# Optimization experiments

Measured on AMD Instinct MI355X. Metric: run time of the kernel, lower is better.

Reference implementation:

```python
import jax, jax.numpy as jnp
import numpy as np

VOCAB, D, B, T = 32000, 1024, 4, 2048

def setup_inputs() -> dict:
    key = jax.random.key(0)
    ks = jax.random.split(key, 7)
    std = 0.01  # model initializes all weights with std=0.01
    return {
        "x": jax.random.randint(ks[0], (B, T), 0, VOCAB),
        "emb_w": jax.random.normal(ks[1], (VOCAB, D), jnp.float32) * std,
        "wq": jax.random.normal(ks[2], (D, D), jnp.float32) * std,
        "wk": jax.random.normal(ks[3], (D, D), jnp.float32) * std,
        "wv": jax.random.normal(ks[4], (D, D), jnp.float32) * std,
        "wo": jax.random.normal(ks[5], (D, D), jnp.float32) * std,
        "wout": jax.random.normal(ks[6], (VOCAB, D), jnp.float32) * std,
    }

def fhe_act(x):
    # polynomial activation: 0.1*x^2 + 0.1*x
    return x * x * 0.1 + x * 0.1

def reference(x, emb_w, wq, wk, wv, wo, wout):
    h = emb_w[x] * 0.01                                 # [B,T,D]
    q = (h @ wq.T) * 0.01                               # [B,T,D]
    k = (h @ wk.T) * 0.01                               # [B,T,D]
    v = (h @ wv.T) * 0.1                                # [B,T,D]
    attn = jnp.einsum('btd,bsd->bts', q, k) * 0.01      # [B,T,T] full (no causal mask)
    attn = fhe_act(attn)
    out = jnp.einsum('bts,bsd->btd', attn, v) * 0.01    # [B,T,D]
    out = (out @ wo.T) * 0.1                            # [B,T,D]
    logits = out @ wout.T                               # [B,T,VOCAB]
    return logits
```

## Files before the change

### kernel.cpp

```cpp
#include <hip/hip_runtime.h>


typedef __bf16 bf16_t;
typedef __bf16 bf16x8 __attribute__((ext_vector_type(8)));
typedef __bf16 bf16x4 __attribute__((ext_vector_type(4)));
typedef float  f32x4  __attribute__((ext_vector_type(4)));

#define VOCAB 32000
#define DIM   1024
#define BATCH 4
#define SEQ   2048
#define BT    (BATCH*SEQ)

__device__ __forceinline__ void gload_lds16(const void* g, void* l) {
    __builtin_amdgcn_global_load_lds(
        (const __attribute__((address_space(1))) void*)g,
        (__attribute__((address_space(3))) void*)l,
        16, 0, 0);
}

__global__ void cast_f32_to_bf16(const float* __restrict__ in, bf16_t* __restrict__ out, int n4) {
    int i = blockIdx.x * blockDim.x + threadIdx.x;
    if (i < n4) {
        float4 v = ((const float4*)in)[i];
        bf16x4 o;
        o.x = (bf16_t)v.x; o.y = (bf16_t)v.y; o.z = (bf16_t)v.z; o.w = (bf16_t)v.w;
        ((bf16x4*)out)[i] = o;
    }
}

__global__ void embed_gather(const int* __restrict__ x, const float* __restrict__ emb,
                             bf16_t* __restrict__ h) {
    const int tok = blockIdx.x;
    const int row = x[tok];
    const float4* src = (const float4*)(emb + (long)row * DIM);
    bf16x4* dst = (bf16x4*)(h + (long)tok * DIM);
    int j = threadIdx.x;
    float4 v = src[j];
    bf16x4 o;
    o.x = (bf16_t)(v.x * 0.01f); o.y = (bf16_t)(v.y * 0.01f);
    o.z = (bf16_t)(v.z * 0.01f); o.w = (bf16_t)(v.w * 0.01f);
    dst[j] = o;
}

template<int ACT, typename CT>
__global__ __launch_bounds__(256) void gemm_bt(
    const bf16_t* __restrict__ A, const bf16_t* __restrict__ B, CT* __restrict__ C,
    int M, int N, int K, long sA, long sB, long sC, float scale)
{
    __shared__ __align__(16) bf16_t lsA[128 * 32];
    __shared__ __align__(16) bf16_t lsB[128 * 32];

    const int bz = blockIdx.z;
    A += (long)bz * sA;  B += (long)bz * sB;  C += (long)bz * sC;

    const int tm = blockIdx.y, tn = blockIdx.x;
    const int t = threadIdx.x;
    const int lane = t & 63, wave = t >> 6;
    const int wm = (wave >> 1) * 64;
    const int wn = (wave & 1) * 64;

    const int srow = t >> 2;
    const int scol = (t & 3) * 8;
    const bf16_t* gA = A + (long)(tm * 128 + srow) * K + scol;
    const bf16_t* gB = B + (long)(tn * 128 + srow) * K + scol;
    bf16_t* lA = &lsA[srow * 32 + scol];
    bf16_t* lB = &lsB[srow * 32 + scol];

    f32x4 acc[4][4];
#pragma unroll
    for (int i = 0; i < 4; ++i)
#pragma unroll
        for (int j = 0; j < 4; ++j)
            acc[i][j] = (f32x4){0.f, 0.f, 0.f, 0.f};

    const int arow = lane & 15;
    const int acol = (lane >> 4) * 8;

    for (int k0 = 0; k0 < K; k0 += 32) {
        __syncthreads();
        gload_lds16(gA + k0,                lA);
        gload_lds16(gA + k0 + 64 * (long)K, lA + 64 * 32);
        gload_lds16(gB + k0,                lB);
        gload_lds16(gB + k0 + 64 * (long)K, lB + 64 * 32);
        __syncthreads();

        bf16x8 af[4], bfr[4];
#pragma unroll
        for (int i = 0; i < 4; ++i) {
            af[i]  = *(const bf16x8*)&lsA[(wm + i * 16 + arow) * 32 + acol];
            bfr[i] = *(const bf16x8*)&lsB[(wn + i * 16 + arow) * 32 + acol];
        }
#pragma unroll
        for (int i = 0; i < 4; ++i)
#pragma unroll
            for (int j = 0; j < 4; ++j)
                acc[i][j] = __builtin_amdgcn_mfma_f32_16x16x32_bf16(af[i], bfr[j], acc[i][j], 0, 0, 0);
    }

    const int crow0 = tm * 128 + wm + (lane >> 4) * 4;
    const int ccol0 = tn * 128 + wn + (lane & 15);
#pragma unroll
    for (int i = 0; i < 4; ++i)
#pragma unroll
        for (int j = 0; j < 4; ++j)
#pragma unroll
            for (int r = 0; r < 4; ++r) {
                float s = acc[i][j][r] * scale;
                if (ACT) s = s * s * 0.1f + s * 0.1f;
                C[(long)(crow0 + i * 16 + r) * N + (ccol0 + j * 16)] = (CT)s;
            }
}

__global__ __launch_bounds__(512, 2) void gemm_bt_256(
    const bf16_t* __restrict__ A, const bf16_t* __restrict__ B, float* __restrict__ C,
    int N, int K, float scale)
{
    __shared__ __align__(16) char smem[131072];
    char* const sm = smem;

    const int lin = blockIdx.x;
    const int xcd = lin & 7, jj = lin >> 3;
    const int tm = xcd * 4 + (jj & 3);
    const int tn = jj >> 2;
    const long trow0 = (long)tm * 256, tcol0 = (long)tn * 256;

    const int tid  = threadIdx.x;
    const int lane = tid & 63;
    const int wave = tid >> 6;
    const int wm = wave >> 2;
    const int wn = wave & 3;
    const int lr = lane & 15;
    const int ko2 = (lane >> 4) * 16;
    const int rbase = lr * 64 + (ko2 ^ (((lr >> 1) & 3) << 4));

    const int o0 = tid * 16, o1 = 8192 + tid * 16;
    int sr0, sc0, sr1, sc1;
    {
        int ol = o0 ^ (((o0 >> 7) & 3) << 4);
        sr0 = ((ol >> 10) >> 1) * 16 + ((ol >> 6) & 15);
        sc0 = ((ol >> 10) & 1) * 32 + ((ol & 63) >> 1);
        ol = o1 ^ (((o1 >> 7) & 3) << 4);
        sr1 = ((ol >> 10) >> 1) * 16 + ((ol >> 6) & 15);
        sc1 = ((ol >> 10) & 1) * 32 + ((ol & 63) >> 1);
    }

    const bf16_t* Abase = A + trow0 * K;
    const bf16_t* Bbase = B + tcol0 * K;

#define STAGE_HT(gbase, kt, half, ldsh) do {                                          \
    gload_lds16((gbase) + (long)((half) * 128 + sr0) * K + ((kt) * 64 + sc0), (ldsh) + o0); \
    gload_lds16((gbase) + (long)((half) * 128 + sr1) * K + ((kt) * 64 + sc1), (ldsh) + o1); \
} while (0)

    f32x4 acc[8][4];
#pragma unroll
    for (int i = 0; i < 8; ++i)
#pragma unroll
        for (int j = 0; j < 4; ++j)
            acc[i][j] = (f32x4){0.f, 0.f, 0.f, 0.f};

#define PHASE(mh, nh, ...) do {                                                       \
    bf16x8 af_[4][2], bv_[2][2];                                                      \
    _Pragma("unroll")                                                                 \
    for (int i_ = 0; i_ < 4; ++i_) {                                                  \
        _Pragma("unroll")                                                             \
        for (int ks_ = 0; ks_ < 2; ++ks_)                                             \
            af_[i_][ks_] = *(const bf16x8*)(ldsA + (mh) * 16384 +                     \
                               ((wm * 4 + i_) * 2 + ks_) * 1024 + rbase);             \
    }                                                                                 \
    _Pragma("unroll")                                                                 \
    for (int j_ = 0; j_ < 2; ++j_) {                                                  \
        _Pragma("unroll")                                                             \
        for (int ks_ = 0; ks_ < 2; ++ks_)                                             \
            bv_[j_][ks_] = *(const bf16x8*)(ldsB + (nh) * 16384 +                     \
                               ((wn * 2 + j_) * 2 + ks_) * 1024 + rbase);             \
    }                                                                                 \
    __VA_ARGS__;                                                                      \
    asm volatile("s_barrier" ::: "memory");                                           \
    asm volatile("s_waitcnt lgkmcnt(0)" ::: "memory");                                \
    __builtin_amdgcn_s_setprio(1);                                                    \
    _Pragma("unroll")                                                                 \
    for (int i_ = 0; i_ < 4; ++i_)                                                    \
        _Pragma("unroll")                                                             \
        for (int j_ = 0; j_ < 2; ++j_)                                                \
            _Pragma("unroll")                                                         \
            for (int ks_ = 0; ks_ < 2; ++ks_)                                         \
                acc[(mh) * 4 + i_][(nh) * 2 + j_] =                                   \
                    __builtin_amdgcn_mfma_f32_16x16x32_bf16(                          \
                        af_[i_][ks_], bv_[j_][ks_],                                   \
                        acc[(mh) * 4 + i_][(nh) * 2 + j_], 0, 0, 0);                  \
    __builtin_amdgcn_s_setprio(0);                                                    \
} while (0)

    {
        char* a0 = sm;
        char* b0 = sm + 32768;
        char* a1 = sm + 65536;
        char* b1 = sm + 65536 + 32768;
        STAGE_HT(Abase, 0, 0, a0);
        STAGE_HT(Bbase, 0, 0, b0);
        STAGE_HT(Abase, 0, 1, a0 + 16384);
        STAGE_HT(Bbase, 0, 1, b0 + 16384);
        STAGE_HT(Abase, 1, 0, a1);
        STAGE_HT(Bbase, 1, 0, b1);
        asm volatile("s_waitcnt vmcnt(4)" ::: "memory");
        asm volatile("s_barrier" ::: "memory");
    }

    const int NT = K / 64;
    for (int t = 0; t < NT; ++t) {
        const int buf = t & 1;
        char* ldsA  = sm + buf * 65536;
        char* ldsB  = ldsA + 32768;
        char* ldsAn = sm + (buf ^ 1) * 65536;
        char* ldsBn = ldsAn + 32768;

        PHASE(0, 0,
              if (t + 1 < NT) {
                  STAGE_HT(Abase, t + 1, 1, ldsAn + 16384);
                  STAGE_HT(Bbase, t + 1, 1, ldsBn + 16384);
              });
        asm volatile("s_barrier" ::: "memory");

        PHASE(0, 1, );
        asm volatile("s_barrier" ::: "memory");

        PHASE(1, 0,
              if (t + 2 < NT) { STAGE_HT(Abase, t + 2, 0, ldsA); });
        asm volatile("s_barrier" ::: "memory");

        PHASE(1, 1,
              if (t + 2 < NT) { STAGE_HT(Bbase, t + 2, 0, ldsB); });
        if (t + 2 < NT) { asm volatile("s_waitcnt vmcnt(4)" ::: "memory"); }
        else            { asm volatile("s_waitcnt vmcnt(0)" ::: "memory"); }
        asm volatile("s_barrier" ::: "memory");
    }

    const int erow = (lane >> 4) * 4;
    const int ecol = lane & 15;
#pragma unroll
    for (int mh = 0; mh < 2; ++mh)
#pragma unroll
        for (int i = 0; i < 4; ++i)
#pragma unroll
            for (int nh = 0; nh < 2; ++nh)
#pragma unroll
                for (int j = 0; j < 2; ++j)
#pragma unroll
                    for (int r = 0; r < 4; ++r) {
                        long row = trow0 + mh * 128 + wm * 64 + i * 16 + erow + r;
                        long col = tcol0 + nh * 128 + wn * 32 + j * 16 + ecol;
                        C[row * N + col] = acc[mh * 4 + i][nh * 2 + j][r] * scale;
                    }
#undef PHASE
#undef STAGE_HT
}

extern "C" void kernel_launch(void* const* d_in, const int* in_sizes, int n_in,
                              void* d_out, int out_size, void* d_ws, size_t ws_size,
                              hipStream_t stream) {
    const int*   x    = (const int*)d_in[0];
    const float* emb  = (const float*)d_in[1];
    const float* wq   = (const float*)d_in[2];
    const float* wk   = (const float*)d_in[3];
    const float* wv   = (const float*)d_in[4];
    const float* wo   = (const float*)d_in[5];
    const float* wout = (const float*)d_in[6];
    float* logits = (float*)d_out;

    char* ws = (char*)d_ws;
    size_t off = 0;
    auto alloc = [&](size_t bytes) {
        char* p = ws + off;
        off += (bytes + 255) & ~(size_t)255;
        return p;
    };
    bf16_t* hb    = (bf16_t*)alloc((size_t)BT * DIM * 2);
    bf16_t* qb    = (bf16_t*)alloc((size_t)BT * DIM * 2);
    bf16_t* kb    = (bf16_t*)alloc((size_t)BT * DIM * 2);
    bf16_t* vtb   = (bf16_t*)alloc((size_t)BATCH * DIM * SEQ * 2);
    bf16_t* attnb = (bf16_t*)alloc((size_t)BATCH * SEQ * SEQ * 2);
    bf16_t* o1b   = (bf16_t*)alloc((size_t)BT * DIM * 2);
    bf16_t* o2b   = (bf16_t*)alloc((size_t)BT * DIM * 2);
    bf16_t* wqb   = (bf16_t*)alloc((size_t)DIM * DIM * 2);
    bf16_t* wkb   = (bf16_t*)alloc((size_t)DIM * DIM * 2);
    bf16_t* wvb   = (bf16_t*)alloc((size_t)DIM * DIM * 2);
    bf16_t* wob   = (bf16_t*)alloc((size_t)DIM * DIM * 2);
    bf16_t* woutb = (bf16_t*)alloc((size_t)VOCAB * DIM * 2);

    {
        int n4 = DIM * DIM / 4;
        cast_f32_to_bf16<<<n4 / 256, 256, 0, stream>>>(wq, wqb, n4);
        cast_f32_to_bf16<<<n4 / 256, 256, 0, stream>>>(wk, wkb, n4);
        cast_f32_to_bf16<<<n4 / 256, 256, 0, stream>>>(wv, wvb, n4);
        cast_f32_to_bf16<<<n4 / 256, 256, 0, stream>>>(wo, wob, n4);
        int n4o = VOCAB * DIM / 4;
        cast_f32_to_bf16<<<n4o / 256, 256, 0, stream>>>(wout, woutb, n4o);
    }

    embed_gather<<<BT, 256, 0, stream>>>(x, emb, hb);

    dim3 blk(256);
    gemm_bt<0, bf16_t><<<dim3(DIM / 128, BT / 128, 1), blk, 0, stream>>>(
        hb, wqb, qb, BT, DIM, DIM, 0, 0, 0, 0.01f);
    gemm_bt<0, bf16_t><<<dim3(DIM / 128, BT / 128, 1), blk, 0, stream>>>(
        hb, wkb, kb, BT, DIM, DIM, 0, 0, 0, 0.01f);
    gemm_bt<0, bf16_t><<<dim3(SEQ / 128, DIM / 128, BATCH), blk, 0, stream>>>(
        wvb, hb, vtb, DIM, SEQ, DIM, 0, (long)SEQ * DIM, (long)DIM * SEQ, 0.1f);
    gemm_bt<1, bf16_t><<<dim3(SEQ / 128, SEQ / 128, BATCH), blk, 0, stream>>>(
        qb, kb, attnb, SEQ, SEQ, DIM,
        (long)SEQ * DIM, (long)SEQ * DIM, (long)SEQ * SEQ, 0.01f);
    gemm_bt<0, bf16_t><<<dim3(DIM / 128, SEQ / 128, BATCH), blk, 0, stream>>>(
        attnb, vtb, o1b, SEQ, DIM, SEQ,
        (long)SEQ * SEQ, (long)DIM * SEQ, (long)SEQ * DIM, 0.01f);
    gemm_bt<0, bf16_t><<<dim3(DIM / 128, BT / 128, 1), blk, 0, stream>>>(
        o1b, wob, o2b, BT, DIM, DIM, 0, 0, 0, 0.1f);

    gemm_bt_256<<<(BT / 256) * (VOCAB / 256), 512, 0, stream>>>(
        o2b, woutb, logits, VOCAB, DIM, 1.0f);
}
```

Before: 997.7 us.

## Reorder GEMM phases by k-substep to reuse B fragments across row halves

The four inner phases of the bf16 MFMA GEMM now iterate over k-substeps and row halves instead of over (row-half, col-half) quadrants. B fragments for all four column blocks are loaded once per k-substep and reused by both A halves, which roughly halves LDS reads per K tile. The prefetch of the next-next tile's A and B half-0 is merged into the final phase. This keeps four B fragments live across phases, which raises register pressure, and it concentrates global-to-LDS issue in one phase.

```diff
diff --git a/kernel.cpp b/kernel.cpp
--- a/kernel.cpp
+++ b/kernel.cpp
@@ -160,22 +160,16 @@
         for (int j = 0; j < 4; ++j)
             acc[i][j] = (f32x4){0.f, 0.f, 0.f, 0.f};
 
-#define PHASE(mh, nh, ...) do {                                                       \
-    bf16x8 af_[4][2], bv_[2][2];                                                      \
-    _Pragma("unroll")                                                                 \
-    for (int i_ = 0; i_ < 4; ++i_) {                                                  \
-        _Pragma("unroll")                                                             \
-        for (int ks_ = 0; ks_ < 2; ++ks_)                                             \
-            af_[i_][ks_] = *(const bf16x8*)(ldsA + (mh) * 16384 +                     \
-                               ((wm * 4 + i_) * 2 + ks_) * 1024 + rbase);             \
-    }                                                                                 \
-    _Pragma("unroll")                                                                 \
-    for (int j_ = 0; j_ < 2; ++j_) {                                                  \
-        _Pragma("unroll")                                                             \
-        for (int ks_ = 0; ks_ < 2; ++ks_)                                             \
-            bv_[j_][ks_] = *(const bf16x8*)(ldsB + (nh) * 16384 +                     \
-                               ((wn * 2 + j_) * 2 + ks_) * 1024 + rbase);             \
-    }                                                                                 \
+#define PHASE_LO(ks, ...) do {                                                        \
+    bf16x8 af_[4];                                                                    \
+    _Pragma("unroll")                                                                 \
+    for (int i_ = 0; i_ < 4; ++i_)                                                    \
+        af_[i_] = *(const bf16x8*)(ldsA +                                             \
+                      ((wm * 4 + i_) * 2 + (ks)) * 1024 + rbase);                     \
+    _Pragma("unroll")                                                                 \
+    for (int c_ = 0; c_ < 4; ++c_)                                                    \
+        bv_[c_] = *(const bf16x8*)(ldsB + (c_ >> 1) * 16384 +                         \
+                      ((wn * 2 + (c_ & 1)) * 2 + (ks)) * 1024 + rbase);               \
     __VA_ARGS__;                                                                      \
     asm volatile("s_barrier" ::: "memory");                                           \
     asm volatile("s_waitcnt lgkmcnt(0)" ::: "memory");                                \
@@ -183,13 +177,28 @@
     _Pragma("unroll")                                                                 \
     for (int i_ = 0; i_ < 4; ++i_)                                                    \
         _Pragma("unroll")                                                             \
-        for (int j_ = 0; j_ < 2; ++j_)                                                \
-            _Pragma("unroll")                                                         \
-            for (int ks_ = 0; ks_ < 2; ++ks_)                                         \
-                acc[(mh) * 4 + i_][(nh) * 2 + j_] =                                   \
-                    __builtin_amdgcn_mfma_f32_16x16x32_bf16(                          \
-                        af_[i_][ks_], bv_[j_][ks_],                                   \
-                        acc[(mh) * 4 + i_][(nh) * 2 + j_], 0, 0, 0);                  \
+        for (int c_ = 0; c_ < 4; ++c_)                                                \
+            acc[i_][c_] = __builtin_amdgcn_mfma_f32_16x16x32_bf16(                    \
+                af_[i_], bv_[c_], acc[i_][c_], 0, 0, 0);                              \
+    __builtin_amdgcn_s_setprio(0);                                                    \
+} while (0)
+
+#define PHASE_HI(ks, ...) do {                                                        \
+    bf16x8 af_[4];                                                                    \
+    _Pragma("unroll")                                                                 \
+    for (int i_ = 0; i_ < 4; ++i_)                                                    \
+        af_[i_] = *(const bf16x8*)(ldsA + 16384 +                                     \
+                      ((wm * 4 + i_) * 2 + (ks)) * 1024 + rbase);                     \
+    __VA_ARGS__;                                                                      \
+    asm volatile("s_barrier" ::: "memory");                                           \
+    asm volatile("s_waitcnt lgkmcnt(0)" ::: "memory");                                \
+    __builtin_amdgcn_s_setprio(1);                                                    \
+    _Pragma("unroll")                                                                 \
+    for (int i_ = 0; i_ < 4; ++i_)                                                    \
+        _Pragma("unroll")                                                             \
+        for (int c_ = 0; c_ < 4; ++c_)                                                \
+            acc[4 + i_][c_] = __builtin_amdgcn_mfma_f32_16x16x32_bf16(                \
+                af_[i_], bv_[c_], acc[4 + i_][c_], 0, 0, 0);                          \
     __builtin_amdgcn_s_setprio(0);                                                    \
 } while (0)
 
@@ -215,23 +224,26 @@
         char* ldsB  = ldsA + 32768;
         char* ldsAn = sm + (buf ^ 1) * 65536;
         char* ldsBn = ldsAn + 32768;
-
-        PHASE(0, 0,
+        bf16x8 bv_[4];
+
+        PHASE_LO(0,
               if (t + 1 < NT) {
                   STAGE_HT(Abase, t + 1, 1, ldsAn + 16384);
                   STAGE_HT(Bbase, t + 1, 1, ldsBn + 16384);
               });
         asm volatile("s_barrier" ::: "memory");
 
-        PHASE(0, 1, );
-        asm volatile("s_barrier" ::: "memory");
-
-        PHASE(1, 0,
-              if (t + 2 < NT) { STAGE_HT(Abase, t + 2, 0, ldsA); });
-        asm volatile("s_barrier" ::: "memory");
-
-        PHASE(1, 1,
-              if (t + 2 < NT) { STAGE_HT(Bbase, t + 2, 0, ldsB); });
+        PHASE_HI(0, );
+        asm volatile("s_barrier" ::: "memory");
+
+        PHASE_LO(1, );
+        asm volatile("s_barrier" ::: "memory");
+
+        PHASE_HI(1,
+              if (t + 2 < NT) {
+                  STAGE_HT(Abase, t + 2, 0, ldsA);
+                  STAGE_HT(Bbase, t + 2, 0, ldsB);
+              });
         if (t + 2 < NT) { asm volatile("s_waitcnt vmcnt(4)" ::: "memory"); }
         else            { asm volatile("s_waitcnt vmcnt(0)" ::: "memory"); }
         asm volatile("s_barrier" ::: "memory");
@@ -240,20 +252,17 @@
     const int erow = (lane >> 4) * 4;
     const int ecol = lane & 15;
 #pragma unroll
-    for (int mh = 0; mh < 2; ++mh)
-#pragma unroll
-        for (int i = 0; i < 4; ++i)
-#pragma unroll
-            for (int nh = 0; nh < 2; ++nh)
-#pragma unroll
-                for (int j = 0; j < 2; ++j)
-#pragma unroll
-                    for (int r = 0; r < 4; ++r) {
-                        long row = trow0 + mh * 128 + wm * 64 + i * 16 + erow + r;
-                        long col = tcol0 + nh * 128 + wn * 32 + j * 16 + ecol;
-                        C[row * N + col] = acc[mh * 4 + i][nh * 2 + j][r] * scale;
-                    }
-#undef PHASE
+    for (int a = 0; a < 8; ++a)
+#pragma unroll
+        for (int c = 0; c < 4; ++c)
+#pragma unroll
+            for (int r = 0; r < 4; ++r) {
+                long row = trow0 + (a >> 2) * 128 + wm * 64 + (a & 3) * 16 + erow + r;
+                long col = tcol0 + (c >> 1) * 128 + wn * 32 + (c & 1) * 16 + ecol;
+                C[row * N + col] = acc[a][c][r] * scale;
+            }
+#undef PHASE_LO
+#undef PHASE_HI
 #undef STAGE_HT
 }
 
```

After: 968.1 us. 1.03x faster.
